# Kernel optimization log

Hardware: AMD Instinct MI355X
Metric: run time of the kernel (lower is better)

## Reference

```python
import jax, jax.numpy as jnp
import numpy as np

N_NODES = 50000
N_EDGES = 800000
D_IN = 128
D_HID = 128
N_CLASSES = 40


def gcn_conv(h, src, dst, W, b, n_nodes):
    """GCNConv: out = D^{-1/2} (A + I) D^{-1/2} (h @ W) + b, with self-loops."""
    h = h @ W  # [N, F_out]
    loop = jnp.arange(n_nodes, dtype=src.dtype)
    s = jnp.concatenate([src, loop])  # [E + N]
    d = jnp.concatenate([dst, loop])
    deg = jax.ops.segment_sum(jnp.ones_like(d, dtype=h.dtype), d, num_segments=n_nodes)
    dinv = jax.lax.rsqrt(jnp.maximum(deg, 1.0))  # deg >= 1 due to self-loops
    norm = dinv[s] * dinv[d]  # [E + N]
    msgs = h[s] * norm[:, None]  # gather: [E + N, F_out]
    out = jax.ops.segment_sum(msgs, d, num_segments=n_nodes)  # scatter-add
    return out + b


def setup_inputs() -> dict:
    key = jax.random.key(0)
    ks = jax.random.split(key, 12)
    x = jax.random.normal(ks[0], (N_NODES, D_IN), dtype=jnp.float32)
    edge_index = jax.random.randint(ks[1], (2, N_EDGES), 0, N_NODES, dtype=jnp.int64)
    def lin(k, fi, fo):
        s = 1.0 / np.sqrt(fi)
        return jax.random.uniform(k, (fi, fo), jnp.float32, -s, s)
    W_pre = lin(ks[2], D_IN, D_HID)
    b_pre = jnp.zeros((D_HID,), jnp.float32)
    W1 = lin(ks[3], D_HID, D_HID)
    b1 = jnp.zeros((D_HID,), jnp.float32)
    W2 = lin(ks[4], D_HID, D_HID)
    b2 = jnp.zeros((D_HID,), jnp.float32)
    W_post = lin(ks[5], D_HID, N_CLASSES)
    b_post = jnp.zeros((N_CLASSES,), jnp.float32)
    return {"x": x, "edge_index": edge_index, "W_pre": W_pre, "b_pre": b_pre,
            "W1": W1, "b1": b1, "W2": W2, "b2": b2,
            "W_post": W_post, "b_post": b_post}


def reference(x, edge_index, W_pre, b_pre, W1, b1, W2, b2, W_post, b_post):
    src, dst = edge_index[0], edge_index[1]
    n = x.shape[0]
    h = x @ W_pre + b_pre                      # pre-process MLP (Linear)
    h = jax.nn.relu(gcn_conv(h, src, dst, W1, b1, n))   # conv1 + act1
    h = jax.nn.relu(gcn_conv(h, src, dst, W2, b2, n))   # conv2 + act2
    return h @ W_post + b_post                 # post-process MLP (Linear)
```

## Files before the change

kernel.cpp:

```cpp
#include <hip/hip_runtime.h>

#define D 128

typedef short bfrag __attribute__((ext_vector_type(8)));
typedef float f32x4 __attribute__((ext_vector_type(4)));
typedef unsigned uint32;

__device__ inline unsigned short bf16_rne(float x) {
    unsigned u = __float_as_uint(x);
    return (unsigned short)((u + 0x7FFFu + ((u >> 16) & 1u)) >> 16);
}
__device__ inline float bf16_to_f(unsigned short h) {
    return __uint_as_float(((unsigned)h) << 16);
}
__device__ inline unsigned split2p(float x) {
    unsigned short hi = bf16_rne(x);
    unsigned short lo = bf16_rne(x - bf16_to_f(hi));
    return (unsigned)hi | ((unsigned)lo << 16);
}

__device__ inline void unpair_r(uint4 q0, uint4 q1, bfrag& ah, bfrag& al) {
    union { uint32 u[4]; bfrag b; } H, L;
    H.u[0] = __builtin_amdgcn_perm(q0.y, q0.x, 0x05040100u);
    H.u[1] = __builtin_amdgcn_perm(q0.w, q0.z, 0x05040100u);
    H.u[2] = __builtin_amdgcn_perm(q1.y, q1.x, 0x05040100u);
    H.u[3] = __builtin_amdgcn_perm(q1.w, q1.z, 0x05040100u);
    L.u[0] = __builtin_amdgcn_perm(q0.y, q0.x, 0x07060302u);
    L.u[1] = __builtin_amdgcn_perm(q0.w, q0.z, 0x07060302u);
    L.u[2] = __builtin_amdgcn_perm(q1.y, q1.x, 0x07060302u);
    L.u[3] = __builtin_amdgcn_perm(q1.w, q1.z, 0x07060302u);
    ah = H.b;
    al = L.b;
}

__device__ inline void split8_r(uint4 q0, uint4 q1, bfrag& ah, bfrag& al) {
    float v[8] = {__uint_as_float(q0.x), __uint_as_float(q0.y), __uint_as_float(q0.z), __uint_as_float(q0.w),
                  __uint_as_float(q1.x), __uint_as_float(q1.y), __uint_as_float(q1.z), __uint_as_float(q1.w)};
    union { unsigned short us[8]; bfrag b; } H, L;
    #pragma unroll
    for (int i = 0; i < 8; i++) {
        unsigned pr = split2p(v[i]);
        H.us[i] = (unsigned short)pr;
        L.us[i] = (unsigned short)(pr >> 16);
    }
    ah = H.b;
    al = L.b;
}

__global__ __launch_bounds__(256) void compose_w(const float* __restrict__ Wpre, const float* __restrict__ W1,
                                                 const float* __restrict__ bpre,
                                                 uint32* __restrict__ wcp, float* __restrict__ bc) {
    int i = blockIdx.x * 256 + threadIdx.x;
    int n = i & 127, k = i >> 7;
    float acc = 0.f;
    #pragma unroll 4
    for (int m = 0; m < 128; m++)
        acc = fmaf(Wpre[k * 128 + m], W1[m * 128 + n], acc);
    wcp[n * 128 + k] = split2p(acc);
    if (i < 128) {
        float b = 0.f;
        #pragma unroll 4
        for (int m = 0; m < 128; m++)
            b = fmaf(bpre[m], W1[m * 128 + i], b);
        bc[i] = b;
    }
}

__global__ __launch_bounds__(256) void deg_raw(const unsigned* __restrict__ raw, int* __restrict__ deg,
                                               int* __restrict__ gmode, unsigned short* __restrict__ csr16,
                                               float* __restrict__ t_c, int E, int Npad, int csrCap4, int nRows,
                                               const float* __restrict__ W2, const float* __restrict__ Wpost,
                                               uint32* __restrict__ w2_p, uint32* __restrict__ wpost_p) {
    __shared__ int smode;
    int gid = blockIdx.x * 256 + threadIdx.x;
    int gstride = gridDim.x * 256;
    int p0 = blockIdx.x * 1024;
    if (threadIdx.x < 64) {
        int p = p0 + threadIdx.x * 16;
        unsigned v = (p < E) ? raw[2 * p + 1] : 0u;
        unsigned long long any = __ballot(v != 0u);
        if (threadIdx.x == 0) smode = (any != 0ull) ? 1 : 0;
    }
    __syncthreads();
    int m = smode;
    if (blockIdx.x == 0 && threadIdx.x == 0) *gmode = m;
    unsigned short sent = (unsigned short)Npad;
    ushort4 s4 = make_ushort4(sent, sent, sent, sent);
    for (int i = gid; i < csrCap4; i += gstride) ((ushort4*)csr16)[i] = s4;
    int sentRows = nRows - Npad;
    int nSentF4 = 8 * sentRows * 4;
    for (int i = gid; i < nSentF4; i += gstride) {
        int chunk = i / (sentRows * 4);
        int rem = i % (sentRows * 4);
        ((float4*)(t_c + (size_t)chunk * nRows * 16 + (size_t)Npad * 16))[rem] = make_float4(0.f, 0.f, 0.f, 0.f);
    }
    for (int i = gid; i < 22528; i += gstride) {
        const float* W; uint32* wp; int idx, ncols;
        if (i < 16384) { W = W2;    wp = w2_p;    idx = i;         ncols = 128; }
        else           { W = Wpost; wp = wpost_p; idx = i - 16384; ncols = 40;  }
        int n = idx >> 7, k = idx & 127;
        float v = (n < ncols) ? W[k * ncols + n] : 0.f;
        wp[idx] = split2p(v);
    }
    int pend = min(p0 + 1024, E);
    for (int p = p0 + threadIdx.x; p < pend; p += 256) {
        int d = m ? (int)raw[E + p] : (int)((const unsigned long long*)raw)[E + p];
        atomicAdd(&deg[d], 1);
    }
}

__global__ __launch_bounds__(256) void rank_block(const int* __restrict__ deg, float* __restrict__ dinv,
                                                  int* __restrict__ local_rank, int* __restrict__ hist_blk, int N) {
    __shared__ int h[256];
    int t = threadIdx.x;
    h[t] = 0;
    __syncthreads();
    int i = blockIdx.x * 256 + t;
    if (i < N) {
        int d = deg[i];
        dinv[i] = 1.0f / sqrtf((float)(d + 1));
        int b = min(d, 255);
        local_rank[i] = atomicAdd(&h[b], 1);
    }
    __syncthreads();
    hist_blk[blockIdx.x * 256 + t] = h[t];
}

__global__ __launch_bounds__(256) void scan_blocks(int* __restrict__ hist_blk, int* __restrict__ binbase,
                                                   int* __restrict__ ebase, int nblk) {
    int b = threadIdx.x;
    int sum = 0;
    int k = 0;
    for (; k + 8 <= nblk; k += 8) {
        int v[8];
        #pragma unroll
        for (int u = 0; u < 8; u++) v[u] = hist_blk[(k + u) * 256 + b];
        #pragma unroll
        for (int u = 0; u < 8; u++) { hist_blk[(k + u) * 256 + b] = sum; sum += v[u]; }
    }
    for (; k < nblk; k++) {
        int v = hist_blk[k * 256 + b];
        hist_blk[k * 256 + b] = sum;
        sum += v;
    }
    __shared__ int s[256], s2[256];
    int bp = (b + 3) & ~3;
    int c = sum, e = sum * bp;
    s[b] = c; s2[b] = e;
    __syncthreads();
    for (int off = 1; off < 256; off <<= 1) {
        int a0 = (b >= off) ? s[b - off] : 0;
        int a1 = (b >= off) ? s2[b - off] : 0;
        __syncthreads();
        s[b] += a0; s2[b] += a1;
        __syncthreads();
    }
    binbase[b] = s[b] - c;
    ebase[b] = s2[b] - e;
}

__global__ __launch_bounds__(256) void emit_perm(const int* __restrict__ deg, const float* __restrict__ dinv,
                                                 const int* __restrict__ local_rank, const int* __restrict__ hist_blk,
                                                 const int* __restrict__ binbase, const int* __restrict__ ebase,
                                                 int* __restrict__ tailcur, int* __restrict__ rowbeg,
                                                 int* __restrict__ cursor, uint4* __restrict__ meta, int N) {
    int i = blockIdx.x * 256 + threadIdx.x;
    if (i >= N) return;
    int d = deg[i];
    int b = min(d, 255);
    int dp = (d + 3) & ~3;
    int rib = hist_blk[blockIdx.x * 256 + b] + local_rank[i];
    int pos = binbase[b] + rib;
    int rb = (b < 255) ? (ebase[b] + rib * ((b + 3) & ~3)) : (ebase[255] + atomicAdd(tailcur, dp));
    rowbeg[i] = rb;
    cursor[i] = 0;
    meta[pos] = make_uint4((unsigned)rb, (unsigned)dp, __float_as_uint(dinv[i]), (unsigned)i);
}

__global__ __launch_bounds__(256) void fill_csr_raw(const unsigned* __restrict__ raw, const int* __restrict__ gmode,
                                                    const int* __restrict__ rowbeg, int* __restrict__ cursor,
                                                    unsigned short* __restrict__ csr16, int E) {
    int e = blockIdx.x * 256 + threadIdx.x;
    if (e >= E) return;
    int m = *gmode;
    int d = m ? (int)raw[E + e] : (int)((const unsigned long long*)raw)[E + e];
    int s = m ? (int)raw[e]     : (int)((const unsigned long long*)raw)[e];
    int pos = atomicAdd(&cursor[d], 1);
    csr16[rowbeg[d] + pos] = (unsigned short)s;
}

template<int EPI, int AFMT>
__global__ __launch_bounds__(512) void gemm_lds(const void* __restrict__ Ap,
                                                const uint32* __restrict__ Wpair,
                                                const float* __restrict__ bias,
                                                const float* __restrict__ dinv,
                                                float* __restrict__ Cf,
                                                uint32* __restrict__ Pout,
                                                int nStrips, int N, int nRows) {
    __shared__ uint32 Wl[128 * 132];
    int tid = threadIdx.x;
    for (int i = tid; i < 16384; i += 512)
        Wl[(i >> 7) * 132 + (i & 127)] = Wpair[i];
    __syncthreads();

    int wave = tid >> 6;
    int lane = tid & 63;
    int l15 = lane & 15, lg = lane >> 4;
    int so = wave >> 1;
    int colbase = (wave & 1) * 64;
    size_t chunkStride = (size_t)nRows * 16;

    const int stride = gridDim.x * 4;
    for (int strip = blockIdx.x * 4 + so; strip < nStrips; strip += stride) {
        int arow = min(strip * 16 + l15, N - 1);
        uint4 cur[8];
        const uint4* p = (const uint4*)Ap + (size_t)arow * 32 + lg * 2;
        #pragma unroll
        for (int ks = 0; ks < 4; ks++) {
            cur[2 * ks]     = p[ks * 8];
            cur[2 * ks + 1] = p[ks * 8 + 1];
        }
        bfrag ah[4], al[4];
        #pragma unroll
        for (int ks = 0; ks < 4; ks++) {
            if (AFMT == 0) unpair_r(cur[2 * ks], cur[2 * ks + 1], ah[ks], al[ks]);
            else           split8_r(cur[2 * ks], cur[2 * ks + 1], ah[ks], al[ks]);
        }
        f32x4 acc[4];
        #pragma unroll
        for (int nt = 0; nt < 4; nt++) acc[nt] = (f32x4){0.f, 0.f, 0.f, 0.f};
        #pragma unroll
        for (int ks = 0; ks < 4; ks++) {
            #pragma unroll
            for (int nt = 0; nt < 4; nt++) {
                const uint32* wp = &Wl[(colbase + nt * 16 + l15) * 132 + ks * 32 + lg * 8];
                uint4 w0 = *(const uint4*)wp;
                uint4 w1 = *(const uint4*)(wp + 4);
                bfrag wh, wl_;
                unpair_r(w0, w1, wh, wl_);
                acc[nt] = __builtin_amdgcn_mfma_f32_16x16x32_bf16(ah[ks], wh, acc[nt], 0, 0, 0);
                acc[nt] = __builtin_amdgcn_mfma_f32_16x16x32_bf16(ah[ks], wl_, acc[nt], 0, 0, 0);
                acc[nt] = __builtin_amdgcn_mfma_f32_16x16x32_bf16(al[ks], wh, acc[nt], 0, 0, 0);
            }
        }
        int row0 = strip * 16;
        if (EPI == 0) {
            float dv[4];
            #pragma unroll
            for (int r = 0; r < 4; r++) dv[r] = dinv[min(row0 + lg * 4 + r, N - 1)];
            #pragma unroll
            for (int nt = 0; nt < 4; nt++) {
                int col = colbase + nt * 16 + l15;
                float bv = bias ? bias[col] : 0.f;
                float* cbase = Cf + (size_t)(col >> 4) * chunkStride + (col & 15);
                #pragma unroll
                for (int r = 0; r < 4; r++)
                    cbase[(size_t)(row0 + lg * 4 + r) * 16] = (acc[nt][r] + bv) * dv[r];
            }
        } else {
            #pragma unroll
            for (int nt = 0; nt < 4; nt++) {
                int col = colbase + nt * 16 + l15;
                float bv = bias[col];
                #pragma unroll
                for (int r = 0; r < 4; r++)
                    Pout[(size_t)(row0 + lg * 4 + r) * D + col] = split2p(acc[nt][r] + bv);
            }
        }
    }
}

__global__ __launch_bounds__(256) void gemm_post(const uint32* __restrict__ P,
                                                 const uint32* __restrict__ Wpair,
                                                 const float* __restrict__ bias,
                                                 float* __restrict__ Cf,
                                                 int nStrips, int N, int outW) {
    int wave = threadIdx.x >> 6;
    int lane = threadIdx.x & 63;
    int l15 = lane & 15, lg = lane >> 4;

    bfrag wh[4][3], wl[4][3];
    #pragma unroll
    for (int ks = 0; ks < 4; ks++)
        #pragma unroll
        for (int nt = 0; nt < 3; nt++) {
            const uint32* wp = Wpair + (size_t)(nt * 16 + l15) * D + ks * 32 + lg * 8;
            uint4 w0 = *(const uint4*)wp;
            uint4 w1 = *(const uint4*)(wp + 4);
            unpair_r(w0, w1, wh[ks][nt], wl[ks][nt]);
        }

    const int stride = gridDim.x * 4;
    for (int strip = blockIdx.x * 4 + wave; strip < nStrips; strip += stride) {
        int arow = min(strip * 16 + l15, N - 1);
        bfrag ah[4], al[4];
        #pragma unroll
        for (int ks = 0; ks < 4; ks++) {
            const uint4* p = (const uint4*)P + (size_t)arow * 32 + lg * 2;
            unpair_r(p[ks * 8], p[ks * 8 + 1], ah[ks], al[ks]);
        }
        f32x4 acc[3];
        #pragma unroll
        for (int nt = 0; nt < 3; nt++) acc[nt] = (f32x4){0.f, 0.f, 0.f, 0.f};
        #pragma unroll
        for (int ks = 0; ks < 4; ks++)
            #pragma unroll
            for (int nt = 0; nt < 3; nt++) {
                acc[nt] = __builtin_amdgcn_mfma_f32_16x16x32_bf16(ah[ks], wh[ks][nt], acc[nt], 0, 0, 0);
                acc[nt] = __builtin_amdgcn_mfma_f32_16x16x32_bf16(ah[ks], wl[ks][nt], acc[nt], 0, 0, 0);
                acc[nt] = __builtin_amdgcn_mfma_f32_16x16x32_bf16(al[ks], wh[ks][nt], acc[nt], 0, 0, 0);
            }
        int row0 = strip * 16;
        #pragma unroll
        for (int nt = 0; nt < 3; nt++) {
            int col = nt * 16 + l15;
            #pragma unroll
            for (int r = 0; r < 4; r++) {
                int row = row0 + lg * 4 + r;
                if (row < N && col < outW)
                    Cf[(size_t)row * outW + col] = acc[nt][r] + bias[col];
            }
        }
    }
}

__global__ __launch_bounds__(256) void gather_xcd(const unsigned short* __restrict__ csr16,
                                                  const uint4* __restrict__ meta,
                                                  const float* __restrict__ t_c, const float* __restrict__ bias,
                                                  uint32* __restrict__ Pout, int N, int nRows) {
    int chunk = blockIdx.x & 7;
    int k = (blockIdx.x >> 3) * 16 + (threadIdx.x >> 4);
    if (k >= N) return;
    uint4 m = meta[k];
    int beg = (int)m.x;
    int degp = (int)m.y;
    float di = __uint_as_float(m.z);
    int node = (int)m.w;
    int w = (threadIdx.x >> 2) & 3;
    int c = threadIdx.x & 3;
    const float* tc = t_c + (size_t)chunk * nRows * 16 + c * 4;
    float4 a0 = make_float4(0.f, 0.f, 0.f, 0.f);
    float4 a1 = make_float4(0.f, 0.f, 0.f, 0.f);
    float4 a2 = make_float4(0.f, 0.f, 0.f, 0.f);
    float4 a3 = make_float4(0.f, 0.f, 0.f, 0.f);
    int end = beg + degp;
    for (int j = beg + 4 * w; j < end; j += 16) {
        ushort4 o = *(const ushort4*)(csr16 + j);
        float4 v0 = *(const float4*)(tc + ((size_t)o.x << 4));
        float4 v1 = *(const float4*)(tc + ((size_t)o.y << 4));
        float4 v2 = *(const float4*)(tc + ((size_t)o.z << 4));
        float4 v3 = *(const float4*)(tc + ((size_t)o.w << 4));
        a0.x += v0.x; a0.y += v0.y; a0.z += v0.z; a0.w += v0.w;
        a1.x += v1.x; a1.y += v1.y; a1.z += v1.z; a1.w += v1.w;
        a2.x += v2.x; a2.y += v2.y; a2.z += v2.z; a2.w += v2.w;
        a3.x += v3.x; a3.y += v3.y; a3.z += v3.z; a3.w += v3.w;
    }
    a0.x += a1.x; a0.y += a1.y; a0.z += a1.z; a0.w += a1.w;
    a2.x += a3.x; a2.y += a3.y; a2.z += a3.z; a2.w += a3.w;
    a0.x += a2.x; a0.y += a2.y; a0.z += a2.z; a0.w += a2.w;
    a0.x += __shfl_xor(a0.x, 4); a0.y += __shfl_xor(a0.y, 4);
    a0.z += __shfl_xor(a0.z, 4); a0.w += __shfl_xor(a0.w, 4);
    a0.x += __shfl_xor(a0.x, 8); a0.y += __shfl_xor(a0.y, 8);
    a0.z += __shfl_xor(a0.z, 8); a0.w += __shfl_xor(a0.w, 8);
    if (w != 0) return;
    float4 tv = *(const float4*)(tc + (size_t)node * 16);
    int col0 = chunk * 16 + c * 4;
    float4 b = *((const float4*)bias + (col0 >> 2));
    float4 r;
    r.x = fmaxf(fmaf(di, a0.x + tv.x, b.x), 0.f);
    r.y = fmaxf(fmaf(di, a0.y + tv.y, b.y), 0.f);
    r.z = fmaxf(fmaf(di, a0.z + tv.z, b.z), 0.f);
    r.w = fmaxf(fmaf(di, a0.w + tv.w, b.w), 0.f);
    uint4 p;
    p.x = split2p(r.x); p.y = split2p(r.y); p.z = split2p(r.z); p.w = split2p(r.w);
    *(uint4*)(Pout + (size_t)node * D + col0) = p;
}

extern "C" void kernel_launch(void* const* d_in, const int* in_sizes, int n_in,
                              void* d_out, int out_size, void* d_ws, size_t ws_size,
                              hipStream_t stream) {
    const float* x      = (const float*)d_in[0];
    const unsigned* edges = (const unsigned*)d_in[1];
    const float* W_pre  = (const float*)d_in[2];
    const float* b_pre  = (const float*)d_in[3];
    const float* W1     = (const float*)d_in[4];
    const float* b1     = (const float*)d_in[5];
    const float* W2     = (const float*)d_in[6];
    const float* b2     = (const float*)d_in[7];
    const float* W_post = (const float*)d_in[8];
    const float* b_post = (const float*)d_in[9];
    float* out = (float*)d_out;

    const int N = in_sizes[0] / D;
    const int E = in_sizes[1] / 2;
    const int nStrips = (N + 15) / 16;
    const int Npad = nStrips * 16;
    const int nRows = Npad + 16;
    const int nBlk = (N + 255) / 256;
    const int csrCap = (E + 4 * N + 255) & ~255;

    char* ws = (char*)d_ws;
    size_t off = 0;
    auto alloc = [&](size_t bytes) { void* p = ws + off; off += (bytes + 255) & ~(size_t)255; return p; };
    uint32* pairA = (uint32*)alloc((size_t)Npad * D * 4);
    uint32* pairB = (uint32*)alloc((size_t)Npad * D * 4);
    float*  bufT  = (float*)alloc((size_t)8 * nRows * 16 * 4);
    float*  dinv    = (float*)alloc((size_t)N * 4);
    int*    deg     = (int*)alloc((size_t)N * 4);
    int*    rowbeg  = (int*)alloc((size_t)N * 4);
    unsigned short* csr16 = (unsigned short*)alloc((size_t)csrCap * 2);
    uint4*  meta    = (uint4*)alloc((size_t)N * 16);
    uint32* wc_p    = (uint32*)alloc(16384 * 4);
    float*  bc      = (float*)alloc(128 * 4);
    uint32* w2_p    = (uint32*)alloc(16384 * 4);
    uint32* wpost_p = (uint32*)alloc(6144 * 4);

    {
        char* t = (char*)bufT;
        size_t toff = 0;
        auto talloc = [&](size_t bytes) { void* p = t + toff; toff += (bytes + 255) & ~(size_t)255; return p; };
        int* cursor     = (int*)talloc((size_t)N * 4);
        int* local_rank = (int*)talloc((size_t)N * 4);
        int* hist_blk   = (int*)talloc((size_t)nBlk * 256 * 4);
        int* mode2      = (int*)talloc(256);
        int* binbase    = (int*)talloc(1024);
        int* ebase      = (int*)talloc(1024);
        int* gmode = mode2;
        int* tailcur = mode2 + 1;

        (void)hipMemsetAsync(mode2, 0, 8, stream);
        (void)hipMemsetAsync(deg, 0, (size_t)N * 4, stream);
        compose_w<<<64, 256, 0, stream>>>(W_pre, W1, b_pre, wc_p, bc);
        deg_raw<<<(E + 1023) / 1024, 256, 0, stream>>>(edges, deg, gmode, csr16, bufT, E, Npad, csrCap / 4, nRows,
                                                       W2, W_post, w2_p, wpost_p);
        rank_block<<<nBlk, 256, 0, stream>>>(deg, dinv, local_rank, hist_blk, N);
        scan_blocks<<<1, 256, 0, stream>>>(hist_blk, binbase, ebase, nBlk);
        emit_perm<<<nBlk, 256, 0, stream>>>(deg, dinv, local_rank, hist_blk, binbase, ebase,
                                            tailcur, rowbeg, cursor, meta, N);
        fill_csr_raw<<<(E + 255) / 256, 256, 0, stream>>>(edges, gmode, rowbeg, cursor, csr16, E);
    }

    const int nGatherBlocks = ((N + 15) / 16) * 8;
    const int gemmGrid = 391;

    gemm_lds<0, 1><<<gemmGrid, 512, 0, stream>>>(x, wc_p, bc, dinv, bufT, nullptr, nStrips, N, nRows);
    gather_xcd<<<nGatherBlocks, 256, 0, stream>>>(csr16, meta, bufT, b1, pairA, N, nRows);

    gemm_lds<0, 0><<<gemmGrid, 512, 0, stream>>>(pairA, w2_p, nullptr, dinv, bufT, nullptr, nStrips, N, nRows);
    gather_xcd<<<nGatherBlocks, 256, 0, stream>>>(csr16, meta, bufT, b2, pairB, N, nRows);

    gemm_post<<<256, 256, 0, stream>>>(pairB, wpost_p, b_post, out, nStrips, N, 40);
}
```

Measured before the change: 268.7 us.

## Fuse graph preprocessing into one cooperative kernel with XCD-partitioned atomics

Replaces the memsets and six preprocessing kernels (weight compose, degree count, rank, scan, permutation, CSR fill) with a single cooperative kernel that uses grid-wide syncs between phases. Edges are first packed into 32-bit src|dst pairs, and the degree and fill atomics are split across 8 block groups by destination range, apparently to keep each atomic target within one XCD's cache. This removes several kernel launches and re-reads of the int64 edge array. In exchange, each grid sync has a cost, every block group scans all edges, and the scan phase runs on a single block while the other 255 wait.

```diff
diff --git a/kernel.cpp b/kernel.cpp
--- a/kernel.cpp
+++ b/kernel.cpp
@@ -1,4 +1,7 @@
 #include <hip/hip_runtime.h>
+#include <hip/hip_cooperative_groups.h>
+
+namespace cg = cooperative_groups;
 
 #define D 128
 
@@ -47,146 +50,171 @@
     al = L.b;
 }
 
-__global__ __launch_bounds__(256) void compose_w(const float* __restrict__ Wpre, const float* __restrict__ W1,
-                                                 const float* __restrict__ bpre,
-                                                 uint32* __restrict__ wcp, float* __restrict__ bc) {
-    int i = blockIdx.x * 256 + threadIdx.x;
-    int n = i & 127, k = i >> 7;
-    float acc = 0.f;
-    #pragma unroll 4
-    for (int m = 0; m < 128; m++)
-        acc = fmaf(Wpre[k * 128 + m], W1[m * 128 + n], acc);
-    wcp[n * 128 + k] = split2p(acc);
-    if (i < 128) {
-        float b = 0.f;
-        #pragma unroll 4
-        for (int m = 0; m < 128; m++)
-            b = fmaf(bpre[m], W1[m * 128 + i], b);
-        bc[i] = b;
-    }
-}
-
-__global__ __launch_bounds__(256) void deg_raw(const unsigned* __restrict__ raw, int* __restrict__ deg,
-                                               int* __restrict__ gmode, unsigned short* __restrict__ csr16,
-                                               float* __restrict__ t_c, int E, int Npad, int csrCap4, int nRows,
-                                               const float* __restrict__ W2, const float* __restrict__ Wpost,
-                                               uint32* __restrict__ w2_p, uint32* __restrict__ wpost_p) {
+struct PrepArgs {
+    const unsigned* raw; unsigned* e32; int* deg; int* tailcur;
+    unsigned short* csr16; float* t_c;
+    int E, N, Npad, csrCap4, nRows, nBlk;
+    const float* W2; const float* Wpost; uint32* w2_p; uint32* wpost_p;
+    const float* Wpre; const float* W1; const float* bpre; uint32* wc_p; float* bc;
+    float* dinv; int* local_rank; int* hist_blk; int* binbase; int* ebase;
+    int* rowbeg; int* cursor; uint4* meta;
+    float scaleDeg, scaleFill;
+};
+
+__global__ __launch_bounds__(256) void prep_all(PrepArgs a) {
+    cg::grid_group grid = cg::this_grid();
+    __shared__ int sh[256], sh2[256];
     __shared__ int smode;
-    int gid = blockIdx.x * 256 + threadIdx.x;
-    int gstride = gridDim.x * 256;
-    int p0 = blockIdx.x * 1024;
-    if (threadIdx.x < 64) {
-        int p = p0 + threadIdx.x * 16;
-        unsigned v = (p < E) ? raw[2 * p + 1] : 0u;
+    int t = threadIdx.x;
+    int gid = blockIdx.x * 256 + t;
+    const int G = gridDim.x * 256;
+
+    if (t < 64) {
+        int p = (int)(((long long)t * a.E) >> 6);
+        unsigned v = a.raw[2 * p + 1];
         unsigned long long any = __ballot(v != 0u);
-        if (threadIdx.x == 0) smode = (any != 0ull) ? 1 : 0;
+        if (t == 0) smode = (any != 0ull) ? 1 : 0;
     }
     __syncthreads();
     int m = smode;
-    if (blockIdx.x == 0 && threadIdx.x == 0) *gmode = m;
-    unsigned short sent = (unsigned short)Npad;
-    ushort4 s4 = make_ushort4(sent, sent, sent, sent);
-    for (int i = gid; i < csrCap4; i += gstride) ((ushort4*)csr16)[i] = s4;
-    int sentRows = nRows - Npad;
+    if (gid == 0) *a.tailcur = 0;
+    for (int i = gid; i < a.N; i += G) a.deg[i] = 0;
+    unsigned short sent = (unsigned short)a.Npad;
+    ushort4 s4v = make_ushort4(sent, sent, sent, sent);
+    for (int i = gid; i < a.csrCap4; i += G) ((ushort4*)a.csr16)[i] = s4v;
+    int sentRows = a.nRows - a.Npad;
     int nSentF4 = 8 * sentRows * 4;
-    for (int i = gid; i < nSentF4; i += gstride) {
+    for (int i = gid; i < nSentF4; i += G) {
         int chunk = i / (sentRows * 4);
         int rem = i % (sentRows * 4);
-        ((float4*)(t_c + (size_t)chunk * nRows * 16 + (size_t)Npad * 16))[rem] = make_float4(0.f, 0.f, 0.f, 0.f);
-    }
-    for (int i = gid; i < 22528; i += gstride) {
+        ((float4*)(a.t_c + (size_t)chunk * a.nRows * 16 + (size_t)a.Npad * 16))[rem] = make_float4(0.f, 0.f, 0.f, 0.f);
+    }
+    for (int i = gid; i < 22528; i += G) {
         const float* W; uint32* wp; int idx, ncols;
-        if (i < 16384) { W = W2;    wp = w2_p;    idx = i;         ncols = 128; }
-        else           { W = Wpost; wp = wpost_p; idx = i - 16384; ncols = 40;  }
+        if (i < 16384) { W = a.W2;    wp = a.w2_p;    idx = i;         ncols = 128; }
+        else           { W = a.Wpost; wp = a.wpost_p; idx = i - 16384; ncols = 40;  }
         int n = idx >> 7, k = idx & 127;
         float v = (n < ncols) ? W[k * ncols + n] : 0.f;
         wp[idx] = split2p(v);
     }
-    int pend = min(p0 + 1024, E);
-    for (int p = p0 + threadIdx.x; p < pend; p += 256) {
-        int d = m ? (int)raw[E + p] : (int)((const unsigned long long*)raw)[E + p];
-        atomicAdd(&deg[d], 1);
-    }
-}
-
-__global__ __launch_bounds__(256) void rank_block(const int* __restrict__ deg, float* __restrict__ dinv,
-                                                  int* __restrict__ local_rank, int* __restrict__ hist_blk, int N) {
-    __shared__ int h[256];
-    int t = threadIdx.x;
-    h[t] = 0;
-    __syncthreads();
-    int i = blockIdx.x * 256 + t;
-    if (i < N) {
-        int d = deg[i];
-        dinv[i] = 1.0f / sqrtf((float)(d + 1));
-        int b = min(d, 255);
-        local_rank[i] = atomicAdd(&h[b], 1);
-    }
-    __syncthreads();
-    hist_blk[blockIdx.x * 256 + t] = h[t];
-}
-
-__global__ __launch_bounds__(256) void scan_blocks(int* __restrict__ hist_blk, int* __restrict__ binbase,
-                                                   int* __restrict__ ebase, int nblk) {
-    int b = threadIdx.x;
-    int sum = 0;
-    int k = 0;
-    for (; k + 8 <= nblk; k += 8) {
-        int v[8];
-        #pragma unroll
-        for (int u = 0; u < 8; u++) v[u] = hist_blk[(k + u) * 256 + b];
-        #pragma unroll
-        for (int u = 0; u < 8; u++) { hist_blk[(k + u) * 256 + b] = sum; sum += v[u]; }
-    }
-    for (; k < nblk; k++) {
-        int v = hist_blk[k * 256 + b];
-        hist_blk[k * 256 + b] = sum;
-        sum += v;
-    }
-    __shared__ int s[256], s2[256];
-    int bp = (b + 3) & ~3;
-    int c = sum, e = sum * bp;
-    s[b] = c; s2[b] = e;
-    __syncthreads();
-    for (int off = 1; off < 256; off <<= 1) {
-        int a0 = (b >= off) ? s[b - off] : 0;
-        int a1 = (b >= off) ? s2[b - off] : 0;
+    for (int i = gid; i < 16384; i += G) {
+        int n = i & 127, k = i >> 7;
+        float acc = 0.f;
+        #pragma unroll 4
+        for (int mm = 0; mm < 128; mm++)
+            acc = fmaf(a.Wpre[k * 128 + mm], a.W1[mm * 128 + n], acc);
+        a.wc_p[n * 128 + k] = split2p(acc);
+        if (i < 128) {
+            float b = 0.f;
+            #pragma unroll 4
+            for (int mm = 0; mm < 128; mm++)
+                b = fmaf(a.bpre[mm], a.W1[mm * 128 + i], b);
+            a.bc[i] = b;
+        }
+    }
+    for (int p = gid; p < a.E; p += G) {
+        int s, d;
+        if (m) { s = (int)a.raw[p]; d = (int)a.raw[a.E + p]; }
+        else   { s = (int)((const unsigned long long*)a.raw)[p]; d = (int)((const unsigned long long*)a.raw)[a.E + p]; }
+        a.e32[p] = (unsigned)s | ((unsigned)d << 16);
+    }
+    __threadfence();
+    grid.sync();
+
+    {
+        int chunk = blockIdx.x & 7;
+        int sub = blockIdx.x >> 3;
+        int estride = (gridDim.x >> 3) * 256;
+        for (int e = sub * 256 + t; e < a.E; e += estride) {
+            int d = (int)(a.e32[e] >> 16);
+            int c = min((int)((float)d * a.scaleDeg), 7);
+            if (c == chunk) atomicAdd(&a.deg[d], 1);
+        }
+    }
+    __threadfence();
+    grid.sync();
+
+    for (int nb = blockIdx.x; nb < a.nBlk; nb += gridDim.x) {
+        sh[t] = 0;
         __syncthreads();
-        s[b] += a0; s2[b] += a1;
+        int i = nb * 256 + t;
+        if (i < a.N) {
+            int d = a.deg[i];
+            a.dinv[i] = 1.0f / sqrtf((float)(d + 1));
+            int b = min(d, 255);
+            a.local_rank[i] = atomicAdd(&sh[b], 1);
+        }
         __syncthreads();
-    }
-    binbase[b] = s[b] - c;
-    ebase[b] = s2[b] - e;
-}
-
-__global__ __launch_bounds__(256) void emit_perm(const int* __restrict__ deg, const float* __restrict__ dinv,
-                                                 const int* __restrict__ local_rank, const int* __restrict__ hist_blk,
-                                                 const int* __restrict__ binbase, const int* __restrict__ ebase,
-                                                 int* __restrict__ tailcur, int* __restrict__ rowbeg,
-                                                 int* __restrict__ cursor, uint4* __restrict__ meta, int N) {
-    int i = blockIdx.x * 256 + threadIdx.x;
-    if (i >= N) return;
-    int d = deg[i];
-    int b = min(d, 255);
-    int dp = (d + 3) & ~3;
-    int rib = hist_blk[blockIdx.x * 256 + b] + local_rank[i];
-    int pos = binbase[b] + rib;
-    int rb = (b < 255) ? (ebase[b] + rib * ((b + 3) & ~3)) : (ebase[255] + atomicAdd(tailcur, dp));
-    rowbeg[i] = rb;
-    cursor[i] = 0;
-    meta[pos] = make_uint4((unsigned)rb, (unsigned)dp, __float_as_uint(dinv[i]), (unsigned)i);
-}
-
-__global__ __launch_bounds__(256) void fill_csr_raw(const unsigned* __restrict__ raw, const int* __restrict__ gmode,
-                                                    const int* __restrict__ rowbeg, int* __restrict__ cursor,
-                                                    unsigned short* __restrict__ csr16, int E) {
-    int e = blockIdx.x * 256 + threadIdx.x;
-    if (e >= E) return;
-    int m = *gmode;
-    int d = m ? (int)raw[E + e] : (int)((const unsigned long long*)raw)[E + e];
-    int s = m ? (int)raw[e]     : (int)((const unsigned long long*)raw)[e];
-    int pos = atomicAdd(&cursor[d], 1);
-    csr16[rowbeg[d] + pos] = (unsigned short)s;
+        a.hist_blk[nb * 256 + t] = sh[t];
+        __syncthreads();
+    }
+    __threadfence();
+    grid.sync();
+
+    if (blockIdx.x == 0) {
+        int b = t;
+        int sum = 0;
+        int k = 0;
+        for (; k + 8 <= a.nBlk; k += 8) {
+            int v[8];
+            #pragma unroll
+            for (int u = 0; u < 8; u++) v[u] = a.hist_blk[(k + u) * 256 + b];
+            #pragma unroll
+            for (int u = 0; u < 8; u++) { a.hist_blk[(k + u) * 256 + b] = sum; sum += v[u]; }
+        }
+        for (; k < a.nBlk; k++) {
+            int v = a.hist_blk[k * 256 + b];
+            a.hist_blk[k * 256 + b] = sum;
+            sum += v;
+        }
+        int bp = (b + 3) & ~3;
+        int c = sum, e = sum * bp;
+        sh[b] = c; sh2[b] = e;
+        __syncthreads();
+        for (int off = 1; off < 256; off <<= 1) {
+            int a0 = (b >= off) ? sh[b - off] : 0;
+            int a1 = (b >= off) ? sh2[b - off] : 0;
+            __syncthreads();
+            sh[b] += a0; sh2[b] += a1;
+            __syncthreads();
+        }
+        a.binbase[b] = sh[b] - c;
+        a.ebase[b] = sh2[b] - e;
+    }
+    __threadfence();
+    grid.sync();
+
+    for (int nb = blockIdx.x; nb < a.nBlk; nb += gridDim.x) {
+        int i = nb * 256 + t;
+        if (i < a.N) {
+            int d = a.deg[i];
+            int b = min(d, 255);
+            int dp = (d + 3) & ~3;
+            int rib = a.hist_blk[nb * 256 + b] + a.local_rank[i];
+            int pos = a.binbase[b] + rib;
+            int rb = (b < 255) ? (a.ebase[b] + rib * ((b + 3) & ~3)) : (a.ebase[255] + atomicAdd(a.tailcur, dp));
+            a.rowbeg[i] = rb;
+            a.cursor[i] = 0;
+            a.meta[pos] = make_uint4((unsigned)rb, (unsigned)dp, __float_as_uint(a.dinv[i]), (unsigned)i);
+        }
+    }
+    __threadfence();
+    grid.sync();
+
+    {
+        int chunk = blockIdx.x & 7;
+        int sub = blockIdx.x >> 3;
+        int estride = (gridDim.x >> 3) * 256;
+        for (int e = sub * 256 + t; e < a.E; e += estride) {
+            unsigned sd = a.e32[e];
+            int d = (int)(sd >> 16);
+            int rb = a.rowbeg[d];
+            int c = min((int)((float)rb * a.scaleFill), 7);
+            if (c != chunk) continue;
+            int pos = atomicAdd(&a.cursor[d], 1);
+            a.csr16[rb + pos] = (unsigned short)(sd & 0xFFFFu);
+        }
+    }
 }
 
 template<int EPI, int AFMT>
@@ -410,35 +438,37 @@
     int*    rowbeg  = (int*)alloc((size_t)N * 4);
     unsigned short* csr16 = (unsigned short*)alloc((size_t)csrCap * 2);
     uint4*  meta    = (uint4*)alloc((size_t)N * 16);
+    unsigned* e32   = (unsigned*)alloc((size_t)E * 4);
     uint32* wc_p    = (uint32*)alloc(16384 * 4);
     float*  bc      = (float*)alloc(128 * 4);
     uint32* w2_p    = (uint32*)alloc(16384 * 4);
     uint32* wpost_p = (uint32*)alloc(6144 * 4);
 
-    {
-        char* t = (char*)bufT;
-        size_t toff = 0;
-        auto talloc = [&](size_t bytes) { void* p = t + toff; toff += (bytes + 255) & ~(size_t)255; return p; };
-        int* cursor     = (int*)talloc((size_t)N * 4);
-        int* local_rank = (int*)talloc((size_t)N * 4);
-        int* hist_blk   = (int*)talloc((size_t)nBlk * 256 * 4);
-        int* mode2      = (int*)talloc(256);
-        int* binbase    = (int*)talloc(1024);
-        int* ebase      = (int*)talloc(1024);
-        int* gmode = mode2;
-        int* tailcur = mode2 + 1;
-
-        (void)hipMemsetAsync(mode2, 0, 8, stream);
-        (void)hipMemsetAsync(deg, 0, (size_t)N * 4, stream);
-        compose_w<<<64, 256, 0, stream>>>(W_pre, W1, b_pre, wc_p, bc);
-        deg_raw<<<(E + 1023) / 1024, 256, 0, stream>>>(edges, deg, gmode, csr16, bufT, E, Npad, csrCap / 4, nRows,
-                                                       W2, W_post, w2_p, wpost_p);
-        rank_block<<<nBlk, 256, 0, stream>>>(deg, dinv, local_rank, hist_blk, N);
-        scan_blocks<<<1, 256, 0, stream>>>(hist_blk, binbase, ebase, nBlk);
-        emit_perm<<<nBlk, 256, 0, stream>>>(deg, dinv, local_rank, hist_blk, binbase, ebase,
-                                            tailcur, rowbeg, cursor, meta, N);
-        fill_csr_raw<<<(E + 255) / 256, 256, 0, stream>>>(edges, gmode, rowbeg, cursor, csr16, E);
-    }
+    char* tws = (char*)bufT;
+    size_t toff = 0;
+    auto talloc = [&](size_t bytes) { void* p = tws + toff; toff += (bytes + 255) & ~(size_t)255; return p; };
+    int* cursor     = (int*)talloc((size_t)N * 4);
+    int* local_rank = (int*)talloc((size_t)N * 4);
+    int* hist_blk   = (int*)talloc((size_t)nBlk * 256 * 4);
+    int* mode2      = (int*)talloc(256);
+    int* binbase    = (int*)talloc(1024);
+    int* ebase      = (int*)talloc(1024);
+    int* tailcur = mode2 + 1;
+
+    PrepArgs pa;
+    pa.raw = edges; pa.e32 = e32; pa.deg = deg; pa.tailcur = tailcur;
+    pa.csr16 = csr16; pa.t_c = bufT;
+    pa.E = E; pa.N = N; pa.Npad = Npad; pa.csrCap4 = csrCap / 4; pa.nRows = nRows; pa.nBlk = nBlk;
+    pa.W2 = W2; pa.Wpost = W_post; pa.w2_p = w2_p; pa.wpost_p = wpost_p;
+    pa.Wpre = W_pre; pa.W1 = W1; pa.bpre = b_pre; pa.wc_p = wc_p; pa.bc = bc;
+    pa.dinv = dinv; pa.local_rank = local_rank; pa.hist_blk = hist_blk;
+    pa.binbase = binbase; pa.ebase = ebase;
+    pa.rowbeg = rowbeg; pa.cursor = cursor; pa.meta = meta;
+    pa.scaleDeg = 8.0f / (float)N;
+    pa.scaleFill = 8.0f / (float)csrCap;
+
+    void* kargs[] = { &pa };
+    (void)hipLaunchCooperativeKernel((const void*)prep_all, dim3(256), dim3(256), kargs, 0, stream);
 
     const int nGatherBlocks = ((N + 15) / 16) * 8;
     const int gemmGrid = 391;
```

Measured after the change: 574.4 us. 114% more time.
